# Performance work log

Hardware: AMD Instinct MI355X
Metric: run time of the kernel (lower is better)

## Reference

```python
import jax, jax.numpy as jnp
import numpy as np


def _gcn_conv(x, src, dst, W, b, n):
    # PyG GCNConv: linear -> add self-loops -> symmetric degree norm -> scatter-add -> bias
    h = x @ W  # [N, out]
    e = src.shape[0]
    loop = jnp.arange(n, dtype=src.dtype)
    s = jnp.concatenate([src, loop])
    d = jnp.concatenate([dst, loop])
    w = jnp.ones(e + n, dtype=x.dtype)
    deg = jax.ops.segment_sum(w, d, num_segments=n)              # in-degree incl. self-loop
    dinv = jnp.where(deg > 0, jax.lax.rsqrt(deg), 0.0)
    norm = dinv[s] * dinv[d]                                     # [E+N]
    out = jax.ops.segment_sum(h[s] * norm[:, None], d, num_segments=n)
    return out + b


def setup_inputs() -> dict:
    key = jax.random.key(0)
    ks = jax.random.split(key, 8)
    N, E = 100000, 1600000
    in_dim, hid, hid1, out_dim = 256, 128, 64, 40
    x = jax.random.normal(ks[0], (N, in_dim), dtype=jnp.float32)
    edge_index = jax.random.randint(ks[1], (2, E), 0, N, dtype=jnp.int32)
    W1 = jax.random.normal(ks[2], (in_dim, hid), dtype=jnp.float32) * (1.0 / np.sqrt(in_dim))
    b1 = jnp.zeros((hid,), jnp.float32)
    W2 = jax.random.normal(ks[3], (hid, hid1), dtype=jnp.float32) * (1.0 / np.sqrt(hid))
    b2 = jnp.zeros((hid1,), jnp.float32)
    Wo = jax.random.normal(ks[4], (hid1, out_dim), dtype=jnp.float32) * (1.0 / np.sqrt(hid1))
    bo = jnp.zeros((out_dim,), jnp.float32)
    return {"x": x, "edge_index": edge_index, "W1": W1, "b1": b1,
            "W2": W2, "b2": b2, "Wo": Wo, "bo": bo}


def reference(x, edge_index, W1, b1, W2, b2, Wo, bo):
    n = x.shape[0]
    src, dst = edge_index[0], edge_index[1]
    h = jax.nn.relu(_gcn_conv(x, src, dst, W1, b1, n))
    # F.dropout(training=False) is identity in inference
    h = _gcn_conv(h, src, dst, W2, b2, n)
    logits = h @ Wo + bo
    return jax.nn.log_softmax(logits, axis=1)
```

## Files before the change

kernel.cpp:

```cpp
#include <hip/hip_runtime.h>
#include <hip/hip_bf16.h>

typedef unsigned short u16;
typedef unsigned int u32;
typedef __attribute__((ext_vector_type(8))) short bf16x8;
typedef __attribute__((ext_vector_type(4))) float f32x4;
typedef __attribute__((ext_vector_type(4))) u16 u16x4;

__device__ __forceinline__ u16 f2bf(float f) {
    __hip_bfloat16 h = __float2bfloat16(f);
    return *reinterpret_cast<u16*>(&h);
}
__device__ __forceinline__ float bf_lo(u32 u) {
    union { u32 u; float f; } v; v.u = u << 16; return v.f;
}
__device__ __forceinline__ float bf_hi(u32 u) {
    union { u32 u; float f; } v; v.u = u & 0xFFFF0000u; return v.f;
}
__device__ __forceinline__ u32 pack2(float a, float b) {
    return (u32)f2bf(a) | ((u32)f2bf(b) << 16);
}

#define NB2 256
#define CHUNK 2048

__global__ void init_kernel(const float* __restrict__ W1, u16* __restrict__ B1, int K1, int N1,
                            const float* __restrict__ W2, u16* __restrict__ B2, int K2, int N2,
                            int* __restrict__ bcur, u32* __restrict__ g1pad,
                            u32* __restrict__ g2pad) {
    int i = blockIdx.x * 256 + threadIdx.x;
    int sz1 = K1 * N1;
    if (i < sz1) {
        int n = i / K1, k = i - n * K1;
        B1[i] = f2bf(W1[(size_t)k * N1 + n]);
    } else if (i - sz1 < K2 * N2) {
        int j = i - sz1;
        int n = j / K2, k = j - n * K2;
        B2[j] = f2bf(W2[(size_t)k * N2 + n]);
    }
    if (blockIdx.x == 0) {
        int t = threadIdx.x;
        bcur[t] = 0;
        if (t < 64) g1pad[t] = 0;
        if (t < 32) g2pad[t] = 0;
    }
}

__launch_bounds__(256)
__global__ void route(const int* __restrict__ src, const int* __restrict__ dst, int E, int R2,
                      int* __restrict__ bcur, int2* __restrict__ bp, int bcap) {
    __shared__ int cnt[NB2];
    __shared__ int cur[NB2];
    const int tid = threadIdx.x;
    const int base = blockIdx.x * CHUNK;
    cnt[tid] = 0;
    __syncthreads();
#pragma unroll
    for (int i = 0; i < CHUNK / 256; i++) {
        int e = base + i * 256 + tid;
        if (e < E) atomicAdd(&cnt[dst[e] / R2], 1);
    }
    __syncthreads();
    {
        int c = cnt[tid];
        cur[tid] = c ? atomicAdd(&bcur[tid], c) : 0;
    }
    __syncthreads();
#pragma unroll
    for (int i = 0; i < CHUNK / 256; i++) {
        int e = base + i * 256 + tid;
        if (e < E) {
            int d = dst[e], s = src[e];
            int b = d / R2;
            int pos = atomicAdd(&cur[b], 1);
            if (pos < bcap) bp[(size_t)b * bcap + pos] = (int2){s, d};
        }
    }
}

__launch_bounds__(256)
__global__ void build_csr(const int2* __restrict__ bp2, const int* __restrict__ bcnt2, int bcap2,
                          int sreg, int R2, int N,
                          int* __restrict__ rs, int* __restrict__ re,
                          float* __restrict__ dinv, int* __restrict__ srcids) {
    __shared__ int2 pl[8300];
    __shared__ int bins[400];
    __shared__ int tsum[256];
    const int b = blockIdx.x;
    const int tid = threadIdx.x;
    const int lo = b * R2;
    int hi = lo + R2; if (hi > N) hi = N;
    const int nb = hi - lo;
    if (nb <= 0) return;
    int cnt = bcnt2[b];
    if (cnt > bcap2) cnt = bcap2;
    const int2* mine = bp2 + (size_t)b * bcap2;

    for (int i = tid; i < nb; i += 256) bins[i] = 0;
    for (int i = tid; i < cnt; i += 256) pl[i] = mine[i];
    __syncthreads();
    for (int i = tid; i < cnt; i += 256) atomicAdd(&bins[pl[i].y - lo], 1);
    __syncthreads();

    const int base4 = tid * 4;
    int creal[4], cpad[4], ex[4];
    int run = 0;
#pragma unroll
    for (int k = 0; k < 4; k++) {
        int idx = base4 + k;
        creal[k] = 0; cpad[k] = 0; ex[k] = 0;
        if (idx < nb) {
            int c = bins[idx];
            creal[k] = c;
            cpad[k] = (c + 3) & ~3;
            dinv[lo + idx] = rsqrtf((float)c + 1.0f);
            ex[k] = run;
            run += cpad[k];
        }
    }
    tsum[tid] = run;
    __syncthreads();
    for (int off = 1; off < 256; off <<= 1) {
        int u = (tid >= off) ? tsum[tid - off] : 0;
        __syncthreads();
        tsum[tid] += u;
        __syncthreads();
    }
    const int toff = ((tid > 0) ? tsum[tid - 1] : 0) + b * sreg;
    __syncthreads();
#pragma unroll
    for (int k = 0; k < 4; k++) {
        int idx = base4 + k;
        if (idx < nb) {
            int st = toff + ex[k];
            bins[idx] = st;
            rs[lo + idx] = st;
            re[lo + idx] = st + cpad[k];
            for (int q = creal[k]; q < cpad[k]; q++) srcids[st + q] = N;
        }
    }
    __syncthreads();
    for (int i = tid; i < cnt; i += 256) {
        int2 p = pl[i];
        int pos = atomicAdd(&bins[p.y - lo], 1);
        srcids[pos] = p.x;
    }
}

template <int BM, int K, int BN, int IFR, int JFR, int WM, int WN, bool ABF16>
__launch_bounds__(256)
__global__ void gemm_mfma(const void* __restrict__ Av, const u16* __restrict__ Bt,
                          const float* __restrict__ dinv, u16* __restrict__ G, int M) {
    constexpr int BK = 32, BKP = 40;
    __shared__ u16 As[BM][BKP];
    __shared__ u16 Bs[BN][BKP];
    const int tid = threadIdx.x;
    const int lane = tid & 63, wave = tid >> 6;
    const int r = lane & 15, g = lane >> 4;
    const int wm = wave % WM, wn = wave / WM;
    const int m0 = blockIdx.x * BM;

    f32x4 acc[IFR][JFR];
#pragma unroll
    for (int i = 0; i < IFR; i++)
#pragma unroll
        for (int j = 0; j < JFR; j++) acc[i][j] = (f32x4){0.f, 0.f, 0.f, 0.f};

    for (int k0 = 0; k0 < K; k0 += BK) {
#pragma unroll
        for (int p = 0; p < BM / 32; p++) {
            int q = tid + p * 256;
            int row = q >> 3, kq = (q & 7) << 2;
            int gr = m0 + row; if (gr >= M) gr = M - 1;
            if constexpr (ABF16) {
                const u16* A = (const u16*)Av;
                *(u16x4*)&As[row][kq] = *(const u16x4*)(A + (size_t)gr * K + k0 + kq);
            } else {
                const float* A = (const float*)Av;
                float4 a = *(const float4*)(A + (size_t)gr * K + k0 + kq);
                u16x4 v = { f2bf(a.x), f2bf(a.y), f2bf(a.z), f2bf(a.w) };
                *(u16x4*)&As[row][kq] = v;
            }
        }
#pragma unroll
        for (int p = 0; p < BN / 32; p++) {
            int q = tid + p * 256;
            int row = q >> 3, kq = (q & 7) << 2;
            *(u16x4*)&Bs[row][kq] = *(const u16x4*)(Bt + (size_t)row * K + k0 + kq);
        }
        __syncthreads();

        bf16x8 af[IFR], bfr[JFR];
#pragma unroll
        for (int i = 0; i < IFR; i++)
            af[i] = *(const bf16x8*)&As[wm * (IFR * 16) + i * 16 + r][g * 8];
#pragma unroll
        for (int j = 0; j < JFR; j++)
            bfr[j] = *(const bf16x8*)&Bs[wn * (JFR * 16) + j * 16 + r][g * 8];
#pragma unroll
        for (int i = 0; i < IFR; i++)
#pragma unroll
            for (int j = 0; j < JFR; j++)
                acc[i][j] = __builtin_amdgcn_mfma_f32_16x16x32_bf16(af[i], bfr[j], acc[i][j], 0, 0, 0);
        __syncthreads();
    }

#pragma unroll
    for (int i = 0; i < IFR; i++) {
#pragma unroll
        for (int t = 0; t < 4; t++) {
            int row = m0 + wm * (IFR * 16) + i * 16 + g * 4 + t;
            if (row < M) {
                float dn = dinv[row];
#pragma unroll
                for (int j = 0; j < JFR; j++) {
                    int col = wn * (JFR * 16) + j * 16 + r;
                    G[(size_t)row * BN + col] = f2bf(acc[i][j][t] * dn);
                }
            }
        }
    }
}

#define ACC8(v) { a0 += bf_lo(v.x); a1 += bf_hi(v.x); a2 += bf_lo(v.y); a3 += bf_hi(v.y); \
                  a4 += bf_lo(v.z); a5 += bf_hi(v.z); a6 += bf_lo(v.w); a7 += bf_hi(v.w); }

__launch_bounds__(256)
__global__ void agg128(const uint4* __restrict__ g1, const float4* __restrict__ bias,
                       const int* __restrict__ rs, const int* __restrict__ re,
                       const int* __restrict__ srcids, const float* __restrict__ dinv,
                       uint4* __restrict__ h1, int n) {
    const int tq = threadIdx.x >> 4;
    const int c  = threadIdx.x & 15;
    const int node = blockIdx.x * 16 + tq;
    if (node >= n) return;
    const float dn = dinv[node];
    uint4 sv = g1[(size_t)node * 16 + c];
    float a0 = bf_lo(sv.x), a1 = bf_hi(sv.x), a2 = bf_lo(sv.y), a3 = bf_hi(sv.y);
    float a4 = bf_lo(sv.z), a5 = bf_hi(sv.z), a6 = bf_lo(sv.w), a7 = bf_hi(sv.w);

    int j = rs[node] >> 2;
    const int jend = re[node] >> 2;
    const int4* ip = (const int4*)srcids;
    if (j < jend) {
        int4 idx = ip[j];
        for (++j; j < jend; ++j) {
            uint4 v0 = g1[(size_t)idx.x * 16 + c];
            uint4 v1 = g1[(size_t)idx.y * 16 + c];
            uint4 v2 = g1[(size_t)idx.z * 16 + c];
            uint4 v3 = g1[(size_t)idx.w * 16 + c];
            int4 nxt = ip[j];
            ACC8(v0); ACC8(v1); ACC8(v2); ACC8(v3);
            idx = nxt;
        }
        uint4 v0 = g1[(size_t)idx.x * 16 + c];
        uint4 v1 = g1[(size_t)idx.y * 16 + c];
        uint4 v2 = g1[(size_t)idx.z * 16 + c];
        uint4 v3 = g1[(size_t)idx.w * 16 + c];
        ACC8(v0); ACC8(v1); ACC8(v2); ACC8(v3);
    }

    float4 b0 = bias[c * 2], b1v = bias[c * 2 + 1];
    uint4 w;
    w.x = pack2(fmaxf(a0 * dn + b0.x, 0.f), fmaxf(a1 * dn + b0.y, 0.f));
    w.y = pack2(fmaxf(a2 * dn + b0.z, 0.f), fmaxf(a3 * dn + b0.w, 0.f));
    w.z = pack2(fmaxf(a4 * dn + b1v.x, 0.f), fmaxf(a5 * dn + b1v.y, 0.f));
    w.w = pack2(fmaxf(a6 * dn + b1v.z, 0.f), fmaxf(a7 * dn + b1v.w, 0.f));
    h1[(size_t)node * 16 + c] = w;
}

__launch_bounds__(256)
__global__ void agg64out(const uint2* __restrict__ g2, const float4* __restrict__ bias,
                         const int* __restrict__ rs, const int* __restrict__ re,
                         const int* __restrict__ srcids, const float* __restrict__ dinv,
                         const float* __restrict__ Wo, const float* __restrict__ bo,
                         float* __restrict__ out, int n) {
    __shared__ float Ws[64 * 40];
    __shared__ float bs[40];
    __shared__ float h2s[16][68];
    for (int i = threadIdx.x; i < 64 * 40; i += 256) Ws[i] = Wo[i];
    if (threadIdx.x < 40) bs[threadIdx.x] = bo[threadIdx.x];

    const int tq = threadIdx.x >> 4;
    const int c  = threadIdx.x & 15;
    const int node = blockIdx.x * 16 + tq;
    if (node < n) {
        const float dn = dinv[node];
        uint2 sv = g2[(size_t)node * 16 + c];
        float a0 = bf_lo(sv.x), a1 = bf_hi(sv.x), a2 = bf_lo(sv.y), a3 = bf_hi(sv.y);
        int j = rs[node] >> 2;
        const int jend = re[node] >> 2;
        const int4* ip = (const int4*)srcids;
        if (j < jend) {
            int4 idx = ip[j];
            for (++j; j < jend; ++j) {
                uint2 v0 = g2[(size_t)idx.x * 16 + c];
                uint2 v1 = g2[(size_t)idx.y * 16 + c];
                uint2 v2 = g2[(size_t)idx.z * 16 + c];
                uint2 v3 = g2[(size_t)idx.w * 16 + c];
                int4 nxt = ip[j];
                a0 += (bf_lo(v0.x) + bf_lo(v1.x)) + (bf_lo(v2.x) + bf_lo(v3.x));
                a1 += (bf_hi(v0.x) + bf_hi(v1.x)) + (bf_hi(v2.x) + bf_hi(v3.x));
                a2 += (bf_lo(v0.y) + bf_lo(v1.y)) + (bf_lo(v2.y) + bf_lo(v3.y));
                a3 += (bf_hi(v0.y) + bf_hi(v1.y)) + (bf_hi(v2.y) + bf_hi(v3.y));
                idx = nxt;
            }
            uint2 v0 = g2[(size_t)idx.x * 16 + c];
            uint2 v1 = g2[(size_t)idx.y * 16 + c];
            uint2 v2 = g2[(size_t)idx.z * 16 + c];
            uint2 v3 = g2[(size_t)idx.w * 16 + c];
            a0 += (bf_lo(v0.x) + bf_lo(v1.x)) + (bf_lo(v2.x) + bf_lo(v3.x));
            a1 += (bf_hi(v0.x) + bf_hi(v1.x)) + (bf_hi(v2.x) + bf_hi(v3.x));
            a2 += (bf_lo(v0.y) + bf_lo(v1.y)) + (bf_lo(v2.y) + bf_lo(v3.y));
            a3 += (bf_hi(v0.y) + bf_hi(v1.y)) + (bf_hi(v2.y) + bf_hi(v3.y));
        }
        float4 bb = bias[c];
        float4 hv = { a0 * dn + bb.x, a1 * dn + bb.y, a2 * dn + bb.z, a3 * dn + bb.w };
        *(float4*)&h2s[tq][c * 4] = hv;
    }
    __syncthreads();

    if (node < n) {
        const int j2 = (c < 8) ? (c + 32) : 39;
        float l0 = bs[c], l1 = bs[c + 16], l2 = bs[j2];
#pragma unroll 8
        for (int k = 0; k < 64; k++) {
            float hk = h2s[tq][k];
            l0 = fmaf(hk, Ws[k * 40 + c], l0);
            l1 = fmaf(hk, Ws[k * 40 + c + 16], l1);
            l2 = fmaf(hk, Ws[k * 40 + j2], l2);
        }
        float m = fmaxf(fmaxf(l0, l1), (c < 8) ? l2 : -3.0e38f);
#pragma unroll
        for (int o = 1; o < 16; o <<= 1) m = fmaxf(m, __shfl_xor(m, o));
        float s = expf(l0 - m) + expf(l1 - m) + ((c < 8) ? expf(l2 - m) : 0.f);
#pragma unroll
        for (int o = 1; o < 16; o <<= 1) s += __shfl_xor(s, o);
        float lse = m + logf(s);
        float* op = out + (size_t)node * 40;
        op[c] = l0 - lse;
        op[c + 16] = l1 - lse;
        if (c < 8) op[c + 32] = l2 - lse;
    }
}

extern "C" void kernel_launch(void* const* d_in, const int* in_sizes, int n_in,
                              void* d_out, int out_size, void* d_ws, size_t ws_size,
                              hipStream_t stream) {
    const float* x  = (const float*)d_in[0];
    const int*   ei = (const int*)d_in[1];
    const float* W1 = (const float*)d_in[2];
    const float* b1 = (const float*)d_in[3];
    const float* W2 = (const float*)d_in[4];
    const float* b2 = (const float*)d_in[5];
    const float* Wo = (const float*)d_in[6];
    const float* bo = (const float*)d_in[7];
    float* out = (float*)d_out;

    const int HID  = in_sizes[3];
    const int IN   = in_sizes[2] / HID;
    const int HID1 = in_sizes[5];
    const int N = in_sizes[0] / IN;
    const int E = in_sizes[1] / 2;
    const int* src = ei;
    const int* dst = ei + E;

    const int R2 = (N + NB2 - 1) / NB2;
    const int bcap2 = E / NB2 + 2048;
    const int sreg  = (bcap2 + 3 * R2 + 32 + 3) & ~3;

    char* ws = (char*)d_ws;
    size_t off = 0;
    auto alloc = [&](size_t bytes) -> void* {
        void* p = ws + off;
        off += (bytes + 255) / 256 * 256;
        return p;
    };
    float* dinv   = (float*)alloc((size_t)N * 4);
    int*   rs     = (int*)alloc((size_t)N * 4);
    int*   re     = (int*)alloc((size_t)N * 4);
    int*   bcur   = (int*)alloc(NB2 * 4);
    int*   srcids = (int*)alloc((size_t)NB2 * sreg * 4);
    u16*   W1t    = (u16*)alloc((size_t)IN * HID * 2);
    u16*   W2t    = (u16*)alloc((size_t)HID * HID1 * 2);
    size_t bp2Bytes = (size_t)NB2 * bcap2 * 8;
    size_t gBytes = (size_t)(N + 1) * HID * 2;
    size_t sharedBytes = (gBytes > bp2Bytes) ? gBytes : bp2Bytes;
    char*  shared = (char*)alloc(sharedBytes);
    int2*  bp2    = (int2*)shared;
    u16*   g1     = (u16*)shared;
    u16*   h1     = (u16*)alloc((size_t)N * HID * 2);
    u16*   g2     = (u16*)alloc((size_t)(N + 1) * HID1 * 2);

    init_kernel<<<(IN * HID + HID * HID1 + 255) / 256, 256, 0, stream>>>(
        W1, W1t, IN, HID, W2, W2t, HID, HID1,
        bcur, (u32*)g1 + (size_t)N * 64, (u32*)g2 + (size_t)N * 32);

    const int nchunk = (E + CHUNK - 1) / CHUNK;
    route<<<nchunk, 256, 0, stream>>>(src, dst, E, R2, bcur, bp2, bcap2);
    build_csr<<<NB2, 256, 0, stream>>>(bp2, bcur, bcap2, sreg, R2, N, rs, re, dinv, srcids);

    const int gblocks = (N + 63) / 64;
    gemm_mfma<64, 256, 128, 2, 4, 2, 2, false><<<gblocks, 256, 0, stream>>>(x, W1t, dinv, g1, N);
    agg128<<<(N + 15) / 16, 256, 0, stream>>>((const uint4*)g1, (const float4*)b1,
                                              rs, re, srcids, dinv, (uint4*)h1, N);

    gemm_mfma<64, 128, 64, 1, 4, 4, 1, true><<<gblocks, 256, 0, stream>>>(h1, W2t, dinv, g2, N);
    agg64out<<<(N + 15) / 16, 256, 0, stream>>>((const uint2*)g2, (const float4*)b2,
                                                rs, re, srcids, dinv, Wo, bo, out, N);

    (void)ws_size; (void)n_in; (void)out_size; (void)HID1;
}
```

Measured before the change: 196.6 us.

## Fuse second-layer GEMM into first aggregation kernel via per-block MFMA

```diff
diff --git a/kernel.cpp b/kernel.cpp
--- a/kernel.cpp
+++ b/kernel.cpp
@@ -226,47 +226,79 @@
                   a4 += bf_lo(v.z); a5 += bf_hi(v.z); a6 += bf_lo(v.w); a7 += bf_hi(v.w); }
 
 __launch_bounds__(256)
-__global__ void agg128(const uint4* __restrict__ g1, const float4* __restrict__ bias,
-                       const int* __restrict__ rs, const int* __restrict__ re,
-                       const int* __restrict__ srcids, const float* __restrict__ dinv,
-                       uint4* __restrict__ h1, int n) {
-    const int tq = threadIdx.x >> 4;
-    const int c  = threadIdx.x & 15;
+__global__ void agg128g2(const uint4* __restrict__ g1, const float4* __restrict__ bias,
+                         const int* __restrict__ rs, const int* __restrict__ re,
+                         const int* __restrict__ srcids, const float* __restrict__ dinv,
+                         const u16* __restrict__ W2t, u16* __restrict__ g2, int n) {
+    __shared__ u32 hq[16][68];
+    const int tid = threadIdx.x;
+    const int lane = tid & 63, wv = tid >> 6;
+    const int tq = tid >> 4;
+    const int c  = tid & 15;
+
+    bf16x8 bfrag[4];
+    {
+        int col = wv * 16 + (lane & 15);
+        int koff = (lane >> 4) * 8;
+#pragma unroll
+        for (int s = 0; s < 4; s++)
+            bfrag[s] = *(const bf16x8*)(W2t + (size_t)col * 128 + s * 32 + koff);
+    }
+
     const int node = blockIdx.x * 16 + tq;
-    if (node >= n) return;
-    const float dn = dinv[node];
-    uint4 sv = g1[(size_t)node * 16 + c];
-    float a0 = bf_lo(sv.x), a1 = bf_hi(sv.x), a2 = bf_lo(sv.y), a3 = bf_hi(sv.y);
-    float a4 = bf_lo(sv.z), a5 = bf_hi(sv.z), a6 = bf_lo(sv.w), a7 = bf_hi(sv.w);
-
-    int j = rs[node] >> 2;
-    const int jend = re[node] >> 2;
-    const int4* ip = (const int4*)srcids;
-    if (j < jend) {
-        int4 idx = ip[j];
-        for (++j; j < jend; ++j) {
+    uint4 w = {0u, 0u, 0u, 0u};
+    if (node < n) {
+        const float dn = dinv[node];
+        uint4 sv = g1[(size_t)node * 16 + c];
+        float a0 = bf_lo(sv.x), a1 = bf_hi(sv.x), a2 = bf_lo(sv.y), a3 = bf_hi(sv.y);
+        float a4 = bf_lo(sv.z), a5 = bf_hi(sv.z), a6 = bf_lo(sv.w), a7 = bf_hi(sv.w);
+
+        int j = rs[node] >> 2;
+        const int jend = re[node] >> 2;
+        const int4* ip = (const int4*)srcids;
+        if (j < jend) {
+            int4 idx = ip[j];
+            for (++j; j < jend; ++j) {
+                uint4 v0 = g1[(size_t)idx.x * 16 + c];
+                uint4 v1 = g1[(size_t)idx.y * 16 + c];
+                uint4 v2 = g1[(size_t)idx.z * 16 + c];
+                uint4 v3 = g1[(size_t)idx.w * 16 + c];
+                int4 nxt = ip[j];
+                ACC8(v0); ACC8(v1); ACC8(v2); ACC8(v3);
+                idx = nxt;
+            }
             uint4 v0 = g1[(size_t)idx.x * 16 + c];
             uint4 v1 = g1[(size_t)idx.y * 16 + c];
             uint4 v2 = g1[(size_t)idx.z * 16 + c];
             uint4 v3 = g1[(size_t)idx.w * 16 + c];
-            int4 nxt = ip[j];
             ACC8(v0); ACC8(v1); ACC8(v2); ACC8(v3);
-            idx = nxt;
-        }
-        uint4 v0 = g1[(size_t)idx.x * 16 + c];
-        uint4 v1 = g1[(size_t)idx.y * 16 + c];
-        uint4 v2 = g1[(size_t)idx.z * 16 + c];
-        uint4 v3 = g1[(size_t)idx.w * 16 + c];
-        ACC8(v0); ACC8(v1); ACC8(v2); ACC8(v3);
-    }
-
-    float4 b0 = bias[c * 2], b1v = bias[c * 2 + 1];
-    uint4 w;
-    w.x = pack2(fmaxf(a0 * dn + b0.x, 0.f), fmaxf(a1 * dn + b0.y, 0.f));
-    w.y = pack2(fmaxf(a2 * dn + b0.z, 0.f), fmaxf(a3 * dn + b0.w, 0.f));
-    w.z = pack2(fmaxf(a4 * dn + b1v.x, 0.f), fmaxf(a5 * dn + b1v.y, 0.f));
-    w.w = pack2(fmaxf(a6 * dn + b1v.z, 0.f), fmaxf(a7 * dn + b1v.w, 0.f));
-    h1[(size_t)node * 16 + c] = w;
+        }
+
+        float4 b0 = bias[c * 2], b1v = bias[c * 2 + 1];
+        w.x = pack2(fmaxf(a0 * dn + b0.x, 0.f), fmaxf(a1 * dn + b0.y, 0.f));
+        w.y = pack2(fmaxf(a2 * dn + b0.z, 0.f), fmaxf(a3 * dn + b0.w, 0.f));
+        w.z = pack2(fmaxf(a4 * dn + b1v.x, 0.f), fmaxf(a5 * dn + b1v.y, 0.f));
+        w.w = pack2(fmaxf(a6 * dn + b1v.z, 0.f), fmaxf(a7 * dn + b1v.w, 0.f));
+    }
+    *(uint4*)&hq[tq][c * 4] = w;
+    __syncthreads();
+
+    const int r = lane & 15, g = lane >> 4;
+    f32x4 acc = (f32x4){0.f, 0.f, 0.f, 0.f};
+#pragma unroll
+    for (int s = 0; s < 4; s++) {
+        bf16x8 af = *(const bf16x8*)&hq[r][s * 16 + g * 4];
+        acc = __builtin_amdgcn_mfma_f32_16x16x32_bf16(af, bfrag[s], acc, 0, 0, 0);
+    }
+#pragma unroll
+    for (int t = 0; t < 4; t++) {
+        int m = g * 4 + t;
+        int nd = blockIdx.x * 16 + m;
+        if (nd < n) {
+            float dn = dinv[nd];
+            g2[(size_t)nd * 64 + wv * 16 + r] = f2bf(acc[t] * dn);
+        }
+    }
 }
 
 __launch_bounds__(256)
@@ -389,7 +421,6 @@
     char*  shared = (char*)alloc(sharedBytes);
     int2*  bp2    = (int2*)shared;
     u16*   g1     = (u16*)shared;
-    u16*   h1     = (u16*)alloc((size_t)N * HID * 2);
     u16*   g2     = (u16*)alloc((size_t)(N + 1) * HID1 * 2);
 
     init_kernel<<<(IN * HID + HID * HID1 + 255) / 256, 256, 0, stream>>>(
@@ -402,10 +433,10 @@
 
     const int gblocks = (N + 63) / 64;
     gemm_mfma<64, 256, 128, 2, 4, 2, 2, false><<<gblocks, 256, 0, stream>>>(x, W1t, dinv, g1, N);
-    agg128<<<(N + 15) / 16, 256, 0, stream>>>((const uint4*)g1, (const float4*)b1,
-                                              rs, re, srcids, dinv, (uint4*)h1, N);
-
-    gemm_mfma<64, 128, 64, 1, 4, 4, 1, true><<<gblocks, 256, 0, stream>>>(h1, W2t, dinv, g2, N);
+
+    agg128g2<<<(N + 15) / 16, 256, 0, stream>>>((const uint4*)g1, (const float4*)b1,
+                                                rs, re, srcids, dinv, W2t, g2, N);
+
     agg64out<<<(N + 15) / 16, 256, 0, stream>>>((const uint2*)g2, (const float4*)b2,
                                                 rs, re, srcids, dinv, Wo, bo, out, N);
 
```

After: 189.5 us, median of 2. 1.04x faster.
